# Kernel optimization log

Measured on AMD Instinct MI355X. Metric: run time of the kernel, lower is better.

Reference implementation:

```python
import jax, jax.numpy as jnp
import numpy as np

W = 128      # windowed_attn_w
H = 8        # num_heads
D = 1024     # model_dim
DK = D // 2  # dim_key = dim_value


def setup_inputs() -> dict:
    key = jax.random.key(0)
    ks = jax.random.split(key, 10)
    B, S = 8, 4096
    qk = jax.random.normal(ks[0], (B, D, S), dtype=jnp.float32)
    v = jax.random.normal(ks[1], (B, D, S), dtype=jnp.float32)
    masks = jnp.ones((B, 1, S), dtype=jnp.float32)
    sc = 1.0 / np.sqrt(D)
    Wq = jax.random.normal(ks[2], (DK, D), dtype=jnp.float32) * sc
    bq = jnp.zeros((DK,), dtype=jnp.float32)
    Wk = jax.random.normal(ks[3], (DK, D), dtype=jnp.float32) * sc
    bk = jnp.zeros((DK,), dtype=jnp.float32)
    Wv = jax.random.normal(ks[4], (DK, D), dtype=jnp.float32) * sc
    bv = jnp.zeros((DK,), dtype=jnp.float32)
    Wo = jax.random.normal(ks[5], (D, DK), dtype=jnp.float32) * (1.0 / np.sqrt(DK))
    bo = jnp.zeros((D,), dtype=jnp.float32)
    return dict(qk=qk, v=v, masks=masks, Wq=Wq, bq=bq, Wk=Wk, bk=bk,
                Wv=Wv, bv=bv, Wo=Wo, bo=bo)


def _to_patches(x):
    # [b, d, s] -> [(b*num_patches), d, W]  (non-overlapping windows)
    b, d, s = x.shape
    np_ = s // W
    return x.reshape(b, d, np_, W).transpose(0, 2, 1, 3).reshape(b * np_, d, W)


def reference(qk, v, masks, Wq, bq, Wk, bk, Wv, bv, Wo, bo):
    B, _, S = qk.shape
    np_ = S // W
    qp = _to_patches(qk)          # [BN, D, W]  (query == key input)
    vp = _to_patches(v)           # [BN, D, W]
    mp = _to_patches(masks)       # [BN, 1, W]  key mask per window

    # 1x1 conv1d projections == channel matmuls
    q = jnp.einsum('ed,bdw->bew', Wq, qp) + bq[:, None]   # [BN, DK, W]
    k = jnp.einsum('ed,bdw->bew', Wk, qp) + bk[:, None]
    val = jnp.einsum('ed,bdw->bew', Wv, vp) + bv[:, None]

    BN = q.shape[0]
    dh = DK // H
    qh = q.reshape(BN, H, dh, W)
    kh = k.reshape(BN, H, dh, W)
    vh = val.reshape(BN, H, dh, W)

    scores = jnp.einsum('bhdi,bhdj->bhij', qh, kh) / jnp.sqrt(jnp.asarray(dh, qh.dtype))
    # mask keys (j axis): [BN,1,W] -> [BN,1,1,W]
    scores = jnp.where(mp[:, :, None, :] > 0, scores, jnp.asarray(-1e9, scores.dtype))
    attn = jax.nn.softmax(scores, axis=-1)
    o = jnp.einsum('bhij,bhdj->bhdi', attn, vh).reshape(BN, DK, W)

    # out_proj: GELU (exact) then 1x1 conv1d DK -> D
    o = jax.nn.gelu(o, approximate=False)
    out = jnp.einsum('de,bew->bdw', Wo, o) + bo[:, None]   # [BN, D, W]

    # undo reshape -> [B, D, S]
    out = out.reshape(B, np_, D, W).transpose(0, 2, 1, 3).reshape(B, D, S)
    out = out * masks
    return out
```

## Files before the change

### kernel.cpp

```cpp
#include <hip/hip_runtime.h>

typedef unsigned short u16b;
typedef __attribute__((ext_vector_type(8))) short short8;
typedef __attribute__((ext_vector_type(4))) float float4v;

#define DEV __device__ __forceinline__

DEV float b2f(u16b u){ union{unsigned int i; float f;} x; x.i=((unsigned int)u)<<16; return x.f; }
DEV u16b f2b(float f){ union{float f; unsigned int i;} x; x.f=f;
  return (u16b)((x.i + 0x7fffu + ((x.i>>16)&1u))>>16); }

DEV void g2l16(const u16b* g, u16b* l){
  __builtin_amdgcn_global_load_lds(
      (const __attribute__((address_space(1))) void*)g,
      (__attribute__((address_space(3))) void*)l, 16, 0, 0);
}

DEV short8 ld8(const void* base, size_t idx, int f){
  if (f) return *(const short8*)((const u16b*)base + idx);
  const float* p = (const float*)base + idx;
  float4v a = *(const float4v*)p;
  float4v b = *(const float4v*)(p+4);
  short8 r;
  r[0]=(short)f2b(a[0]); r[1]=(short)f2b(a[1]); r[2]=(short)f2b(a[2]); r[3]=(short)f2b(a[3]);
  r[4]=(short)f2b(b[0]); r[5]=(short)f2b(b[1]); r[6]=(short)f2b(b[2]); r[7]=(short)f2b(b[3]);
  return r;
}

__global__ void sniff_k(const void* __restrict__ qk, int* __restrict__ flag){
  const u16b* u = (const u16b*)qk;
  int t = threadIdx.x;
  u16b x = u[(size_t)2*t*257];
  int e = (x>>7)&0xFF;
  int ok = (e>=100 && e<=134 && (x&0x7FFF)!=0) ? 1 : 0;
  unsigned long long b = __ballot(ok);
  __shared__ int cnt[4];
  if ((t&63)==0) cnt[t>>6] = __popcll(b);
  __syncthreads();
  if (t==0) *flag = (cnt[0]+cnt[1]+cnt[2]+cnt[3] >= 128) ? 1 : 0;
}

struct IngestArgs {
  const void* src[9];
  int n[9];
  int off[9];
};

__global__ __launch_bounds__(256)
void ingest_k(IngestArgs a, u16b* __restrict__ dst, const int* __restrict__ flag){
  const int f = *flag;
  const int stride = gridDim.x*blockDim.x;
#pragma unroll
  for (int t=0;t<9;t++){
    const void* s = a.src[t];
    int n = a.n[t], o = a.off[t];
    for (int i = blockIdx.x*blockDim.x + threadIdx.x; i < n; i += stride){
      float v = f ? b2f(((const u16b*)s)[i]) : ((const float*)s)[i];
      dst[o + i] = f2b(v);
    }
  }
}

__global__ __launch_bounds__(256,4)
void transpose2_k(const void* __restrict__ qk, const void* __restrict__ vv,
                  u16b* __restrict__ outq, u16b* __restrict__ outv,
                  const int* __restrict__ flag)
{
  __shared__ unsigned int X[4][2080];
  const int f = *flag;
  const int R = 1024, C = 4096;
  const int z = blockIdx.z;
  const void* in = (z<8) ? qk : vv;
  u16b* out = (z<8) ? outq : outv;
  const int zz = z&7;
  const int c0 = blockIdx.x*256;
  const int r0 = blockIdx.y*64;
  const size_t base = (size_t)zz * (size_t)R * (size_t)C;
  const int t = threadIdx.x;
  const int r2 = t>>3, c8 = t&7;
  const size_t ra = base + (size_t)(r0 + 2*r2    )*C + c0 + c8*8;
  const size_t rb = base + (size_t)(r0 + 2*r2 + 1)*C + c0 + c8*8;

  if (f){
    const u16b* p = (const u16b*)in;
    short8 va[4], vb[4];
#pragma unroll
    for (int tt=0;tt<4;tt++) va[tt] = *(const short8*)(p + ra + tt*64);
#pragma unroll
    for (int tt=0;tt<4;tt++) vb[tt] = *(const short8*)(p + rb + tt*64);
#pragma unroll
    for (int tt=0;tt<4;tt++)
#pragma unroll
      for (int k=0;k<8;k++){
        unsigned int w = (((unsigned int)(unsigned short)vb[tt][k])<<16)
                       |  (unsigned int)(unsigned short)va[tt][k];
        X[tt][r2*65 + c8*8 + k] = w;
      }
  } else {
    const float* p = (const float*)in;
    float4v a[4][2], b[4][2];
#pragma unroll
    for (int tt=0;tt<4;tt++){
      a[tt][0] = *(const float4v*)(p + ra + tt*64);
      a[tt][1] = *(const float4v*)(p + ra + tt*64 + 4);
    }
#pragma unroll
    for (int tt=0;tt<4;tt++){
      b[tt][0] = *(const float4v*)(p + rb + tt*64);
      b[tt][1] = *(const float4v*)(p + rb + tt*64 + 4);
    }
#pragma unroll
    for (int tt=0;tt<4;tt++)
#pragma unroll
      for (int k=0;k<8;k++){
        float fa = a[tt][k>>2][k&3];
        float fb = b[tt][k>>2][k&3];
        unsigned int w = (((unsigned int)f2b(fb))<<16)
                       |  (unsigned int)f2b(fa);
        X[tt][r2*65 + c8*8 + k] = w;
      }
  }
  __syncthreads();
#pragma unroll
  for (int tt=0;tt<4;tt++)
#pragma unroll
    for (int i=0;i<2;i++){
      int idx = i*256 + t;
      int c = idx>>3, rq = idx&7;
      unsigned int d0 = X[tt][(4*rq+0)*65 + c];
      unsigned int d1 = X[tt][(4*rq+1)*65 + c];
      unsigned int d2 = X[tt][(4*rq+2)*65 + c];
      unsigned int d3 = X[tt][(4*rq+3)*65 + c];
      uint4 o; o.x=d0; o.y=d1; o.z=d2; o.w=d3;
      *(uint4*)&out[base + (size_t)(c0 + tt*64 + c)*R + r0 + 8*rq] = o;
    }
}

template<int MODE>
__global__ __launch_bounds__(256,2)
void gemm_kt(const u16b* __restrict__ A, const u16b* __restrict__ B,
             void* __restrict__ Cv, const u16b* __restrict__ bias,
             const u16b* __restrict__ mask, const int* __restrict__ flag,
             int M, int N, int K)
{
  __shared__ __align__(16) u16b a_sh[4096];
  __shared__ __align__(16) u16b b_sh[4096];
  const int f = (MODE==2) ? *flag : 0;
  const int tid  = threadIdx.x;
  const int lane = tid & 63;
  const int wv   = tid >> 6;
  const int wm   = (wv>>1)*64, wn = (wv&1)*64;
  const int q    = lane>>4, ln = lane&15;
  const int m0   = blockIdx.y*128, n0 = blockIdx.x*128;

  const int L0 = wv*64 + lane;
  const int r0s = L0>>2;
  const int kc0 = (L0&3) ^ ((r0s>>1)&3);
  const int L1 = (wv+4)*64 + lane;
  const int r1s = L1>>2;
  const int kc1 = (L1&3) ^ ((r1s>>1)&3);
  const size_t ga0 = (size_t)(m0+r0s)*K + (kc0<<3);
  const size_t ga1 = (size_t)(m0+r1s)*K + (kc1<<3);
  const size_t gb0 = (size_t)(n0+r0s)*K + (kc0<<3);
  const size_t gb1 = (size_t)(n0+r1s)*K + (kc1<<3);

  const int sw  = (q ^ ((ln>>1)&3))<<3;
  const int aoff = (wm+ln)*32 + sw;
  const int boff = (wn+ln)*32 + sw;

  float4v acc[4][4];
#pragma unroll
  for (int i=0;i<4;i++)
#pragma unroll
    for (int j=0;j<4;j++) acc[i][j] = float4v{0.f,0.f,0.f,0.f};

  for (int k0=0; k0<K; k0+=32){
    __syncthreads();
    g2l16(&A[ga0 + k0], &a_sh[wv*512]);
    g2l16(&A[ga1 + k0], &a_sh[(wv+4)*512]);
    g2l16(&B[gb0 + k0], &b_sh[wv*512]);
    g2l16(&B[gb1 + k0], &b_sh[(wv+4)*512]);
    asm volatile("s_waitcnt vmcnt(0)" ::: "memory");
    __syncthreads();
    short8 af[4], bfr[4];
#pragma unroll
    for (int mt=0;mt<4;mt++) af[mt]  = *(const short8*)&a_sh[aoff + mt*512];
#pragma unroll
    for (int nt=0;nt<4;nt++) bfr[nt] = *(const short8*)&b_sh[boff + nt*512];
#pragma unroll
    for (int mt=0;mt<4;mt++)
#pragma unroll
      for (int nt=0;nt<4;nt++)
        acc[mt][nt] = __builtin_amdgcn_mfma_f32_16x16x32_bf16(
            af[mt], bfr[nt], acc[mt][nt], 0,0,0);
  }

#pragma unroll
  for (int mt=0;mt<4;mt++)
#pragma unroll
    for (int nt=0;nt<4;nt++)
#pragma unroll
      for (int r=0;r<4;r++){
        int gm = m0 + wm + mt*16 + q*4 + r;
        int gn = n0 + wn + nt*16 + ln;
        float v = acc[mt][nt][r];
        if (MODE==3) v += b2f(bias[gn]);
        else         v += b2f(bias[gm]);
        if (MODE==2){
          v *= b2f(mask[gn]);
          size_t oidx = ((size_t)(gn>>12)*1024 + gm)*4096 + (gn&4095);
          if (f) ((u16b*)Cv)[oidx] = f2b(v);
          else   ((float*)Cv)[oidx] = v;
        } else if (MODE==3){
          u16b* dst = (u16b*)Cv + ((size_t)(gn>>9)<<24);
          dst[(size_t)gm*512 + (gn&511)] = f2b(v);
        } else {
          ((u16b*)Cv)[(size_t)gm*N + gn] = f2b(v);
        }
      }
}

__global__ __launch_bounds__(256,2)
void attn_k(const u16b* __restrict__ QT, const u16b* __restrict__ KT,
            const u16b* __restrict__ V2, const u16b* __restrict__ mask,
            u16b* __restrict__ GT)
{
  __shared__ u16b v_sh[64][136];
  __shared__ u16b p_sh[4][32][136];
  const int bid = blockIdx.x;
  const int w = bid>>3, h = bid&7;
  const int tid = threadIdx.x, lane = tid&63, wv = tid>>6;
  const int q = lane>>4, ln = lane&15;
  const size_t cb = (size_t)w*128;

#pragma unroll
  for (int i=0;i<4;i++){
    int idx=i*256+tid, row=idx>>4, ch=(idx&15)*8;
    *(short8*)&v_sh[row][ch] =
        *(const short8*)&V2[(size_t)(h*64+row)*32768 + cb + ch];
  }

  short8 qf[2][2], kf[8][2];
#pragma unroll
  for (int mt=0;mt<2;mt++)
#pragma unroll
    for (int ks=0;ks<2;ks++)
      qf[mt][ks] = *(const short8*)&QT[(cb + wv*32 + mt*16 + ln)*512 + h*64 + ks*32 + q*8];
#pragma unroll
  for (int nt=0;nt<8;nt++)
#pragma unroll
    for (int ks=0;ks<2;ks++)
      kf[nt][ks] = *(const short8*)&KT[(cb + nt*16 + ln)*512 + h*64 + ks*32 + q*8];

  float4v sa[2][8];
#pragma unroll
  for (int mt=0;mt<2;mt++)
#pragma unroll
    for (int nt=0;nt<8;nt++) sa[mt][nt] = float4v{0.f,0.f,0.f,0.f};
#pragma unroll
  for (int ks=0;ks<2;ks++)
#pragma unroll
    for (int mt=0;mt<2;mt++)
#pragma unroll
      for (int nt=0;nt<8;nt++)
        sa[mt][nt] = __builtin_amdgcn_mfma_f32_16x16x32_bf16(
            qf[mt][ks], kf[nt][ks], sa[mt][nt], 0,0,0);

  float mk[8];
#pragma unroll
  for (int nt=0;nt<8;nt++) mk[nt] = b2f(mask[cb + nt*16 + ln]);
#pragma unroll
  for (int mt=0;mt<2;mt++)
#pragma unroll
    for (int nt=0;nt<8;nt++)
#pragma unroll
      for (int r=0;r<4;r++){
        float s = sa[mt][nt][r]*0.125f;
        sa[mt][nt][r] = (mk[nt] > 0.0f) ? s : -1e9f;
      }

  float mrow[2][4], lrow[2][4];
#pragma unroll
  for (int mt=0;mt<2;mt++)
#pragma unroll
    for (int r=0;r<4;r++){
      float m = -3e38f;
#pragma unroll
      for (int nt=0;nt<8;nt++) m = fmaxf(m, sa[mt][nt][r]);
#pragma unroll
      for (int d=1; d<16; d<<=1) m = fmaxf(m, __shfl_xor(m, d));
      mrow[mt][r] = m;
    }
#pragma unroll
  for (int mt=0;mt<2;mt++)
#pragma unroll
    for (int nt=0;nt<8;nt++)
#pragma unroll
      for (int r=0;r<4;r++)
        sa[mt][nt][r] = __expf(sa[mt][nt][r] - mrow[mt][r]);
#pragma unroll
  for (int mt=0;mt<2;mt++)
#pragma unroll
    for (int r=0;r<4;r++){
      float l = 0.f;
#pragma unroll
      for (int nt=0;nt<8;nt++) l += sa[mt][nt][r];
#pragma unroll
      for (int d=1; d<16; d<<=1) l += __shfl_xor(l, d);
      lrow[mt][r] = l;
    }

#pragma unroll
  for (int mt=0;mt<2;mt++)
#pragma unroll
    for (int nt=0;nt<8;nt++)
#pragma unroll
      for (int r=0;r<4;r++)
        p_sh[wv][mt*16 + q*4 + r][nt*16 + ln] = f2b(sa[mt][nt][r]);
  __syncthreads();

  float4v oa[2][4];
#pragma unroll
  for (int mt=0;mt<2;mt++)
#pragma unroll
    for (int nt=0;nt<4;nt++) oa[mt][nt] = float4v{0.f,0.f,0.f,0.f};
#pragma unroll
  for (int ks=0;ks<4;ks++){
    short8 pf[2], vf[4];
#pragma unroll
    for (int mt=0;mt<2;mt++) pf[mt] = *(const short8*)&p_sh[wv][mt*16+ln][ks*32+q*8];
#pragma unroll
    for (int nt=0;nt<4;nt++) vf[nt] = *(const short8*)&v_sh[nt*16+ln][ks*32+q*8];
#pragma unroll
    for (int mt=0;mt<2;mt++)
#pragma unroll
      for (int nt=0;nt<4;nt++)
        oa[mt][nt] = __builtin_amdgcn_mfma_f32_16x16x32_bf16(
            pf[mt], vf[nt], oa[mt][nt], 0,0,0);
  }

#pragma unroll
  for (int mt=0;mt<2;mt++)
#pragma unroll
    for (int nt=0;nt<4;nt++)
#pragma unroll
      for (int r=0;r<4;r++){
        float x = oa[mt][nt][r] * (1.0f / lrow[mt][r]);
        float g = 0.5f * x * (1.0f + erff(x * 0.70710678118f));
        GT[(cb + wv*32 + mt*16 + q*4 + r)*512 + h*64 + nt*16 + ln] = f2b(g);
      }
}

extern "C" void kernel_launch(void* const* d_in, const int* in_sizes, int n_in,
                              void* d_out, int out_size, void* d_ws, size_t ws_size,
                              hipStream_t stream)
{
  const void* qk    = d_in[0];
  const void* v     = d_in[1];
  const void* masks = d_in[2];

  char* ws = (char*)d_ws;
  int*  flag  = (int*)ws;
  u16b* wbase = (u16b*)(ws + 1024);
  const int OWQ=0, OWK=524288, OWV=1048576, OWO=1572864;
  const int OBQ=2097152, OBK=2097664, OBV=2098176, OBO=2098688, OMSK=2099712;

  u16b* QT  = (u16b*)(ws + ((size_t)  8<<20));
  u16b* KT  = (u16b*)(ws + ((size_t) 40<<20));
  u16b* V2  = (u16b*)(ws + ((size_t) 72<<20));
  u16b* Xtq = (u16b*)(ws + ((size_t)104<<20));
  u16b* Xtv = (u16b*)(ws + ((size_t)168<<20));
  u16b* GT  = KT;

  sniff_k<<<1,256,0,stream>>>(qk, flag);

  IngestArgs ia;
  ia.src[0]=d_in[3]; ia.n[0]=524288; ia.off[0]=OWQ;
  ia.src[1]=d_in[5]; ia.n[1]=524288; ia.off[1]=OWK;
  ia.src[2]=d_in[7]; ia.n[2]=524288; ia.off[2]=OWV;
  ia.src[3]=d_in[9]; ia.n[3]=524288; ia.off[3]=OWO;
  ia.src[4]=d_in[4]; ia.n[4]=512;    ia.off[4]=OBQ;
  ia.src[5]=d_in[6]; ia.n[5]=512;    ia.off[5]=OBK;
  ia.src[6]=d_in[8]; ia.n[6]=512;    ia.off[6]=OBV;
  ia.src[7]=d_in[10];ia.n[7]=1024;   ia.off[7]=OBO;
  ia.src[8]=masks;   ia.n[8]=32768;  ia.off[8]=OMSK;
  ingest_k<<<1024,256,0,stream>>>(ia, wbase, flag);

  transpose2_k<<<dim3(16,16,16),256,0,stream>>>(qk, v, Xtq, Xtv, flag);
  gemm_kt<3><<<dim3(8,256),256,0,stream>>>(Xtq, wbase+OWQ, QT, wbase+OBQ, nullptr, flag, 32768, 1024, 1024);
  gemm_kt<1><<<dim3(256,4),256,0,stream>>>(wbase+OWV, Xtv, V2, wbase+OBV, nullptr, flag, 512, 32768, 1024);
  attn_k<<<2048,256,0,stream>>>(QT, KT, V2, wbase+OMSK, GT);
  gemm_kt<2><<<dim3(256,8),256,0,stream>>>(wbase+OWO, GT, d_out, wbase+OBO, wbase+OMSK, flag, 1024, 32768, 512);
}
```

Before: 584.4 us.

## Fuse qk transpose into QK projection GEMM with register-prefetched A tiles

Replaces the separate transpose of the qk input plus the transposed-A GEMM with a single projection kernel. It reads the raw [B,D,S] activations directly, converts and transposes them through LDS into a swizzled A tile, and prefetches the next K-slice into registers. This removes a full write and re-read of the transposed qk buffer, which is about 64MB of bf16 traffic. In exchange it adds extra LDS round trips and barriers per K step, and the tile is 128x128 over K=1024 with a grouped block order. The v transpose stays as its own kernel.

```diff
diff --git a/kernel.cpp b/kernel.cpp
--- a/kernel.cpp
+++ b/kernel.cpp
@@ -62,20 +62,16 @@
 }
 
 __global__ __launch_bounds__(256,4)
-void transpose2_k(const void* __restrict__ qk, const void* __restrict__ vv,
-                  u16b* __restrict__ outq, u16b* __restrict__ outv,
+void transpose1_k(const void* __restrict__ in, u16b* __restrict__ out,
                   const int* __restrict__ flag)
 {
   __shared__ unsigned int X[4][2080];
   const int f = *flag;
-  const int R = 1024, C = 4096;
-  const int z = blockIdx.z;
-  const void* in = (z<8) ? qk : vv;
-  u16b* out = (z<8) ? outq : outv;
-  const int zz = z&7;
+  const int C = 4096;
+  const int zz = blockIdx.z;
   const int c0 = blockIdx.x*256;
   const int r0 = blockIdx.y*64;
-  const size_t base = (size_t)zz * (size_t)R * (size_t)C;
+  const size_t base = (size_t)zz * (size_t)1024 * (size_t)C;
   const int t = threadIdx.x;
   const int r2 = t>>3, c8 = t&7;
   const size_t ra = base + (size_t)(r0 + 2*r2    )*C + c0 + c8*8;
@@ -132,8 +128,168 @@
       unsigned int d2 = X[tt][(4*rq+2)*65 + c];
       unsigned int d3 = X[tt][(4*rq+3)*65 + c];
       uint4 o; o.x=d0; o.y=d1; o.z=d2; o.w=d3;
-      *(uint4*)&out[base + (size_t)(c0 + tt*64 + c)*R + r0 + 8*rq] = o;
-    }
+      *(uint4*)&out[base + (size_t)(c0 + tt*64 + c)*1024 + r0 + 8*rq] = o;
+    }
+}
+
+DEV void loadA_f32(const float* __restrict__ src, int k0, int r2, int c8, int s0,
+                   float4v (&F)[8]){
+#pragma unroll
+  for (int st=0;st<2;st++)
+#pragma unroll
+    for (int j=0;j<2;j++)
+#pragma unroll
+      for (int h=0;h<2;h++)
+        F[st*4+j*2+h] = *(const float4v*)&src[(size_t)(k0+2*r2+j)*4096
+                                              + s0 + st*64 + c8*8 + h*4];
+}
+
+DEV void loadA_bf16(const u16b* __restrict__ src, int k0, int r2, int c8, int s0,
+                    short8 (&H)[4]){
+#pragma unroll
+  for (int st=0;st<2;st++)
+#pragma unroll
+    for (int j=0;j<2;j++)
+      H[st*2+j] = *(const short8*)&src[(size_t)(k0+2*r2+j)*4096
+                                       + s0 + st*64 + c8*8];
+}
+
+template<bool BF>
+DEV void proj_step(const void* __restrict__ qkv, size_t bbase,
+                   const u16b* __restrict__ Wqk,
+                   int k0, int kn, int n0, int s0,
+                   int t, int lane, int wv, int q, int ln, int r2, int c8,
+                   int wm, int wn,
+                   float4v (&Fc)[8], short8 (&Hc)[4],
+                   float4v (&Fn)[8], short8 (&Hn)[4],
+                   unsigned int (*X)[2088],
+                   u16b* __restrict__ a_sh, u16b* __restrict__ b_sh,
+                   float4v (&acc)[4][4])
+{
+  __syncthreads();
+  if (BF) loadA_bf16((const u16b*)qkv + bbase, kn, r2, c8, s0, Hn);
+  else    loadA_f32 ((const float*)qkv + bbase, kn, r2, c8, s0, Fn);
+#pragma unroll
+  for (int pp=0; pp<4; pp++){
+    int r = (pp*4+wv)*8 + (lane>>3);
+    int g = lane&7;
+    g2l16(&Wqk[(size_t)(n0+r)*1024 + k0 + ((g ^ ((r>>1)&7))<<3)],
+          &b_sh[(pp*4+wv)*512]);
+  }
+#pragma unroll
+  for (int st=0;st<2;st++)
+#pragma unroll
+    for (int k=0;k<8;k++){
+      unsigned int w;
+      if (BF) w = (((unsigned int)(unsigned short)Hc[st*2+1][k])<<16)
+                |  (unsigned int)(unsigned short)Hc[st*2+0][k];
+      else    w = (((unsigned int)f2b(Fc[st*4+2+(k>>2)][k&3]))<<16)
+                |  (unsigned int)f2b(Fc[st*4+0+(k>>2)][k&3]);
+      X[st][r2*65 + c8*8 + k] = w;
+    }
+  __syncthreads();
+#pragma unroll
+  for (int st=0;st<2;st++)
+#pragma unroll
+    for (int i=0;i<2;i++){
+      int idx = i*256 + t;
+      int c = idx>>3, rq = idx&7;
+      unsigned int d0 = X[st][(4*rq+0)*65 + c];
+      unsigned int d1 = X[st][(4*rq+1)*65 + c];
+      unsigned int d2 = X[st][(4*rq+2)*65 + c];
+      unsigned int d3 = X[st][(4*rq+3)*65 + c];
+      int s = st*64 + c;
+      uint4 o; o.x=d0; o.y=d1; o.z=d2; o.w=d3;
+      *(uint4*)&a_sh[s*64 + ((rq ^ ((s>>1)&7))<<3)] = o;
+    }
+  asm volatile("s_waitcnt vmcnt(0)" ::: "memory");
+  __syncthreads();
+#pragma unroll
+  for (int k2=0;k2<2;k2++){
+    short8 af[4], bf[4];
+#pragma unroll
+    for (int mt=0;mt<4;mt++){
+      int row = wm + mt*16 + ln;
+      af[mt] = *(const short8*)&a_sh[row*64 + (((k2*4+q) ^ ((row>>1)&7))<<3)];
+    }
+#pragma unroll
+    for (int nf=0;nf<4;nf++){
+      int row = wn + nf*16 + ln;
+      bf[nf] = *(const short8*)&b_sh[row*64 + (((k2*4+q) ^ ((row>>1)&7))<<3)];
+    }
+#pragma unroll
+    for (int mt=0;mt<4;mt++)
+#pragma unroll
+      for (int nf=0;nf<4;nf++)
+        acc[mt][nf] = __builtin_amdgcn_mfma_f32_16x16x32_bf16(
+            af[mt], bf[nf], acc[mt][nf], 0,0,0);
+  }
+}
+
+__global__ __launch_bounds__(256,2)
+void proj_qk_k(const void* __restrict__ qkv, const u16b* __restrict__ Wqk,
+               u16b* __restrict__ QT, const u16b* __restrict__ bias,
+               const int* __restrict__ flag)
+{
+  __shared__ unsigned int X[2][2088];
+  __shared__ __align__(16) u16b a_sh[8192];
+  __shared__ __align__(16) u16b b_sh[8192];
+
+  const int flat = blockIdx.x;
+  const int p  = ((flat>>6)<<3) + (flat&7);
+  const int nt = (flat>>3)&7;
+  const int m0 = p*128, n0 = nt*128;
+  const size_t bbase = (size_t)(m0>>12) * (size_t)(1024*4096);
+  const int s0 = m0 & 4095;
+  const int t = threadIdx.x, lane = t&63, wv = t>>6;
+  const int q = lane>>4, ln = lane&15;
+  const int r2 = t>>3, c8 = t&7;
+  const int wm = (wv>>1)*64, wn = (wv&1)*64;
+
+  float4v acc[4][4];
+#pragma unroll
+  for (int i=0;i<4;i++)
+#pragma unroll
+    for (int j=0;j<4;j++) acc[i][j] = float4v{0.f,0.f,0.f,0.f};
+
+  float4v F0[8], F1[8]; short8 H0[4], H1[4];
+  const int f = *flag;
+  if (f){
+    loadA_bf16((const u16b*)qkv + bbase, 0, r2, c8, s0, H0);
+    for (int kk=0; kk<16; kk+=2){
+      int k0 = kk*64;
+      proj_step<true>(qkv, bbase, Wqk, k0,      (k0+ 64<1024)?k0+ 64:0, n0, s0,
+                      t, lane, wv, q, ln, r2, c8, wm, wn,
+                      F0, H0, F1, H1, X, a_sh, b_sh, acc);
+      proj_step<true>(qkv, bbase, Wqk, k0+64,   (k0+128<1024)?k0+128:0, n0, s0,
+                      t, lane, wv, q, ln, r2, c8, wm, wn,
+                      F1, H1, F0, H0, X, a_sh, b_sh, acc);
+    }
+  } else {
+    loadA_f32((const float*)qkv + bbase, 0, r2, c8, s0, F0);
+    for (int kk=0; kk<16; kk+=2){
+      int k0 = kk*64;
+      proj_step<false>(qkv, bbase, Wqk, k0,      (k0+ 64<1024)?k0+ 64:0, n0, s0,
+                       t, lane, wv, q, ln, r2, c8, wm, wn,
+                       F0, H0, F1, H1, X, a_sh, b_sh, acc);
+      proj_step<false>(qkv, bbase, Wqk, k0+64,   (k0+128<1024)?k0+128:0, n0, s0,
+                       t, lane, wv, q, ln, r2, c8, wm, wn,
+                       F1, H1, F0, H0, X, a_sh, b_sh, acc);
+    }
+  }
+
+#pragma unroll
+  for (int mt=0;mt<4;mt++)
+#pragma unroll
+    for (int nf=0;nf<4;nf++)
+#pragma unroll
+      for (int r=0;r<4;r++){
+        int gm = m0 + wm + mt*16 + q*4 + r;
+        int gn = n0 + wn + nf*16 + ln;
+        float v = acc[mt][nf][r] + b2f(bias[gn]);
+        u16b* dst = QT + ((size_t)(gn>>9)<<24);
+        dst[(size_t)gm*512 + (gn&511)] = f2b(v);
+      }
 }
 
 template<int MODE>
@@ -204,16 +360,12 @@
         int gm = m0 + wm + mt*16 + q*4 + r;
         int gn = n0 + wn + nt*16 + ln;
         float v = acc[mt][nt][r];
-        if (MODE==3) v += b2f(bias[gn]);
-        else         v += b2f(bias[gm]);
+        v += b2f(bias[gm]);
         if (MODE==2){
           v *= b2f(mask[gn]);
           size_t oidx = ((size_t)(gn>>12)*1024 + gm)*4096 + (gn&4095);
           if (f) ((u16b*)Cv)[oidx] = f2b(v);
           else   ((float*)Cv)[oidx] = v;
-        } else if (MODE==3){
-          u16b* dst = (u16b*)Cv + ((size_t)(gn>>9)<<24);
-          dst[(size_t)gm*512 + (gn&511)] = f2b(v);
         } else {
           ((u16b*)Cv)[(size_t)gm*N + gn] = f2b(v);
         }
@@ -368,7 +520,6 @@
   u16b* QT  = (u16b*)(ws + ((size_t)  8<<20));
   u16b* KT  = (u16b*)(ws + ((size_t) 40<<20));
   u16b* V2  = (u16b*)(ws + ((size_t) 72<<20));
-  u16b* Xtq = (u16b*)(ws + ((size_t)104<<20));
   u16b* Xtv = (u16b*)(ws + ((size_t)168<<20));
   u16b* GT  = KT;
 
@@ -386,8 +537,8 @@
   ia.src[8]=masks;   ia.n[8]=32768;  ia.off[8]=OMSK;
   ingest_k<<<1024,256,0,stream>>>(ia, wbase, flag);
 
-  transpose2_k<<<dim3(16,16,16),256,0,stream>>>(qk, v, Xtq, Xtv, flag);
-  gemm_kt<3><<<dim3(8,256),256,0,stream>>>(Xtq, wbase+OWQ, QT, wbase+OBQ, nullptr, flag, 32768, 1024, 1024);
+  transpose1_k<<<dim3(16,16,8),256,0,stream>>>(v, Xtv, flag);
+  proj_qk_k<<<2048,256,0,stream>>>(qk, wbase+OWQ, QT, wbase+OBQ, flag);
   gemm_kt<1><<<dim3(256,4),256,0,stream>>>(wbase+OWV, Xtv, V2, wbase+OBV, nullptr, flag, 512, 32768, 1024);
   attn_k<<<2048,256,0,stream>>>(QT, KT, V2, wbase+OMSK, GT);
   gemm_kt<2><<<dim3(256,8),256,0,stream>>>(wbase+OWO, GT, d_out, wbase+OBO, wbase+OMSK, flag, 1024, 32768, 512);
```

New measurement: 579.0 us. About the same (-0.9%).
